# Performance work log

Measured on AMD Instinct MI355X. Metric: run time of the kernel, lower is better.

Reference implementation:

```python
import jax, jax.numpy as jnp
import numpy as np

NUM_HEADS = 16
PROJECT_DIM = 1024
HEAD_DIM = PROJECT_DIM // NUM_HEADS  # 64; used only for the softmax scale


def setup_inputs() -> dict:
    key = jax.random.key(0)
    k1, k2, k3 = jax.random.split(key, 3)
    B, N, D = 8, 3072, PROJECT_DIM
    inputs = jax.random.normal(k1, (B, N, D), dtype=jnp.float32)
    wqkv = jax.random.normal(k2, (D, 3 * D), dtype=jnp.float32) * (1.0 / np.sqrt(D))
    dense_w = jax.random.normal(k3, (3 * D, D), dtype=jnp.float32) * (1.0 / np.sqrt(3 * D))
    dense_b = jnp.zeros((D,), dtype=jnp.float32)
    return {"inputs": inputs, "wqkv": wqkv, "dense_w": dense_w, "dense_b": dense_b}


def reference(inputs, wqkv, dense_w, dense_b):
    B, N, D = inputs.shape
    H = NUM_HEADS
    # fused QKV projection: [B, N, 3D]
    qkv = jnp.einsum('bnd,de->bne', inputs, wqkv)
    # separate heads: [B, H, N, 3*head_dim]
    qkv = qkv.reshape(B, N, H, (3 * D) // H).transpose(0, 2, 1, 3)
    # NOTE: faithful to source — split along TOKEN axis (axis=2) into 3 chunks
    q, k, v = jnp.split(qkv, 3, axis=2)  # each [B, H, N//3, 3*head_dim]
    scale = 1.0 / jnp.sqrt(jnp.float32(HEAD_DIM))
    logits = jnp.einsum('bhqc,bhkc->bhqk', q, k) * scale  # [B, H, N//3, N//3]
    attn = jax.nn.softmax(logits, axis=-1)
    out = jnp.einsum('bhqk,bhkc->bhqc', attn, v)  # [B, H, N//3, 3*head_dim]
    # recombine heads -> [B, N//3, 3D]
    out = out.transpose(0, 2, 1, 3).reshape(B, N // 3, 3 * D)
    # output projection -> [B, N//3, D]
    return jnp.einsum('bnc,cd->bnd', out, dense_w) + dense_b
```

## Files before the change

### kernel.cpp

```cpp
#include <hip/hip_runtime.h>
#include <hip/hip_bf16.h>

typedef unsigned short u16;
using f32x4  = __attribute__((ext_vector_type(4))) float;
using bf16x8 = __attribute__((ext_vector_type(8))) short;

typedef __attribute__((address_space(1))) const void global_cvoid;
typedef __attribute__((address_space(3))) void lds_void;

__device__ __forceinline__ void async16(const u16* g, u16* l) {
    __builtin_amdgcn_global_load_lds((global_cvoid*)g, (lds_void*)l, 16, 0, 0);
}

__device__ __forceinline__ u16 f2bf(float f) {
    union { float f; unsigned u; } cv; cv.f = f;
    unsigned r = cv.u + 0x7fff + ((cv.u >> 16) & 1);
    return (u16)(r >> 16);
}

__device__ __forceinline__ u16 f2bf_rz(float f) {
    union { float f; unsigned u; } cv; cv.f = f;
    return (u16)(cv.u >> 16);
}

__device__ __forceinline__ float dppmax16(float x) {
    union { float f; int i; } c, o;
    c.f = x;
    o.i = __builtin_amdgcn_update_dpp(0, c.i, 0xB1,  0xF, 0xF, true); c.f = fmaxf(c.f, o.f);
    o.i = __builtin_amdgcn_update_dpp(0, c.i, 0x4E,  0xF, 0xF, true); c.f = fmaxf(c.f, o.f);
    o.i = __builtin_amdgcn_update_dpp(0, c.i, 0x141, 0xF, 0xF, true); c.f = fmaxf(c.f, o.f);
    o.i = __builtin_amdgcn_update_dpp(0, c.i, 0x140, 0xF, 0xF, true); c.f = fmaxf(c.f, o.f);
    return c.f;
}

__global__ __launch_bounds__(256) void cast_kernel(const float* __restrict__ src,
                                                   u16* __restrict__ dst, int n4) {
    int i = blockIdx.x * blockDim.x + threadIdx.x;
    int st = gridDim.x * blockDim.x;
    for (; i < n4; i += st) {
        float4 v = ((const float4*)src)[i];
        ushort4 o;
        o.x = f2bf(v.x); o.y = f2bf(v.y); o.z = f2bf(v.z); o.w = f2bf(v.w);
        ((ushort4*)dst)[i] = o;
    }
}

__global__ __launch_bounds__(256) void wtrans_kernel(const float* __restrict__ src,
                                                     u16* __restrict__ dst, int R, int C) {
    __shared__ float tile[64][68];
    int ct = blockIdx.x, rt = blockIdx.y;
    int t = threadIdx.x;
    int r = t >> 2;
    const float* s = src + (size_t)(rt * 64 + r) * C + ct * 64;
#pragma unroll
    for (int jj = 0; jj < 4; ++jj) {
        int c4 = (t & 3) + jj * 4;
        float4 v = *(const float4*)(s + c4 * 4);
        *(float4*)&tile[r][c4 * 4] = v;
    }
    __syncthreads();
    int od = t >> 2;
    u16* d = dst + (size_t)(ct * 64 + od) * R + rt * 64;
#pragma unroll
    for (int jj = 0; jj < 4; ++jj) {
        int c4 = (t & 3) + jj * 4;
        ushort4 v;
        v.x = f2bf(tile[c4 * 4 + 0][od]);
        v.y = f2bf(tile[c4 * 4 + 1][od]);
        v.z = f2bf(tile[c4 * 4 + 2][od]);
        v.w = f2bf(tile[c4 * 4 + 3][od]);
        *(ushort4*)(d + c4 * 4) = v;
    }
}

template<bool OUT_F32>
__global__ __launch_bounds__(256, 2)
void gemm_bt_kernel(const u16* __restrict__ A, const u16* __restrict__ BT,
                    void* __restrict__ Cout, const float* __restrict__ bias,
                    u16* __restrict__ VTout,
                    int M, int N, int K) {
    __shared__ u16 lA[128 * 64];
    __shared__ u16 lB[128 * 64];
    const int t = threadIdx.x;
    const int w = t >> 6, lane = t & 63;
    const int nbx = N >> 7;
    const int nwg = gridDim.x;
    int bid = blockIdx.x;
    int cpx = nwg >> 3;
    int swz = (bid & 7) * cpx + (bid >> 3);
    const int bx = swz % nbx;
    const int by = swz / nbx;
    const size_t m0 = (size_t)by * 128, n0 = (size_t)bx * 128;

    const int lr = lane >> 3;
    const int lc = (lane & 7) * 8;
    const int wr = (w >> 1) * 64, wc = (w & 1) * 64;

    f32x4 acc[4][4] = {};

    for (int kk = 0; kk < K; kk += 64) {
        __syncthreads();
#pragma unroll
        for (int i = 0; i < 4; ++i) {
            int rr = (w * 4 + i) * 8 + lr;
            async16(A  + (m0 + rr) * (size_t)K + kk + lc, &lA[(w * 4 + i) * 512]);
            async16(BT + (n0 + rr) * (size_t)K + kk + lc, &lB[(w * 4 + i) * 512]);
        }
        __syncthreads();
#pragma unroll
        for (int ks = 0; ks < 2; ++ks) {
            bf16x8 af[4], bfv[4];
#pragma unroll
            for (int m = 0; m < 4; ++m)
                af[m] = *(const bf16x8*)&lA[(wr + m * 16 + (lane & 15)) * 64 + ks * 32 + (lane >> 4) * 8];
#pragma unroll
            for (int n = 0; n < 4; ++n)
                bfv[n] = *(const bf16x8*)&lB[(wc + n * 16 + (lane & 15)) * 64 + ks * 32 + (lane >> 4) * 8];
#pragma unroll
            for (int m = 0; m < 4; ++m)
#pragma unroll
                for (int n = 0; n < 4; ++n)
                    acc[m][n] = __builtin_amdgcn_mfma_f32_16x16x32_bf16(af[m], bfv[n], acc[m][n], 0, 0, 0);
        }
    }

    const int r0 = (lane >> 4) * 4;
    const int cl = lane & 15;
    if constexpr (OUT_F32) {
        float* C = (float*)Cout;
#pragma unroll
        for (int m = 0; m < 4; ++m) {
            size_t row = m0 + wr + m * 16 + r0;
#pragma unroll
            for (int n = 0; n < 4; ++n) {
                size_t col = n0 + wc + n * 16 + cl;
                float bv = bias[col];
#pragma unroll
                for (int r = 0; r < 4; ++r)
                    C[(row + r) * (size_t)N + col] = acc[m][n][r] + bv;
            }
        }
    } else {
        u16* C = (u16*)Cout;
#pragma unroll
        for (int m = 0; m < 4; ++m) {
            size_t row = m0 + wr + m * 16 + r0;
#pragma unroll
            for (int n = 0; n < 4; ++n) {
                size_t col = n0 + wc + n * 16 + cl;
#pragma unroll
                for (int r = 0; r < 4; ++r)
                    C[(row + r) * (size_t)N + col] = f2bf(acc[m][n][r]);
            }
        }
    }
}

__global__ __launch_bounds__(512, 2)
void gemm256_kernel(const u16* __restrict__ A, const u16* __restrict__ BT,
                    u16* __restrict__ Cout, u16* __restrict__ VTout,
                    int M, int N, int K) {
    __shared__ u16 lds[65536];
    u16* lA = lds;
    u16* lB = lds + 32768;

    const int t = threadIdx.x, w = t >> 6, l = t & 63;
    const int g = l >> 4, ql = l & 15;
    const int wm = w >> 2, wn = w & 3;
    const int nbx = N >> 8;
    int bid = blockIdx.x;
    int cpx = gridDim.x >> 3;
    int swz = (bid & 7) * cpx + (bid >> 3);
    const int bx = swz % nbx, by = swz / nbx;
    const size_t m0 = (size_t)by * 256, n0 = (size_t)bx * 256;

    const u16* Ag = A  + m0 * (size_t)K;
    const u16* Bg = BT + n0 * (size_t)K;

    unsigned soff[2];
#pragma unroll
    for (int i = 0; i < 2; ++i) {
        int ch = i * 512 + t;
        int r = ch >> 2, c = ch & 3;
        soff[i] = (unsigned)(r * K + (c ^ ((r >> 1) & 3)) * 8);
    }

#define STAGE8(kh3) do {                                                           \
    int sl_ = (kh3) & 3;                                                           \
    _Pragma("unroll")                                                              \
    for (int i = 0; i < 2; ++i) {                                                  \
        async16(Ag + soff[i] + (unsigned)(kh3) * 32u, lA + sl_ * 8192 + (i * 512 + w * 64) * 8); \
        async16(Bg + soff[i] + (unsigned)(kh3) * 32u, lB + sl_ * 8192 + (i * 512 + w * 64) * 8); \
    } } while (0)

    STAGE8(0); STAGE8(1); STAGE8(2);

    f32x4 acc[8][4] = {};
    const int cswz = (g ^ ((ql >> 1) & 3)) * 8;
    const int arow = wm * 128 + ql;
    const int brow = wn * 64 + ql;

    auto phase = [&](int kh, int vm, bool st) {
        if (vm == 8)      asm volatile("s_waitcnt vmcnt(8)" ::: "memory");
        else if (vm == 4) asm volatile("s_waitcnt vmcnt(4)" ::: "memory");
        else              asm volatile("s_waitcnt vmcnt(0)" ::: "memory");
        __builtin_amdgcn_s_barrier();
        const u16* sA = lA + (kh & 3) * 8192;
        const u16* sB = lB + (kh & 3) * 8192;
        bf16x8 fa[8], fb[4];
#pragma unroll
        for (int m = 0; m < 8; ++m)
            fa[m] = *(const bf16x8*)&sA[(arow + m * 16) * 32 + cswz];
#pragma unroll
        for (int n = 0; n < 4; ++n)
            fb[n] = *(const bf16x8*)&sB[(brow + n * 16) * 32 + cswz];
        if (st) STAGE8(kh + 3);
        __builtin_amdgcn_s_setprio(1);
#pragma unroll
        for (int m = 0; m < 8; ++m)
#pragma unroll
            for (int n = 0; n < 4; ++n)
                acc[m][n] = __builtin_amdgcn_mfma_f32_16x16x32_bf16(fa[m], fb[n], acc[m][n], 0, 0, 0);
        __builtin_amdgcn_s_setprio(0);
    };

    const int KH = K >> 5;
#pragma unroll 1
    for (int kh = 0; kh < KH - 3; ++kh) phase(kh, 8, true);
    phase(KH - 3, 8, false);
    phase(KH - 2, 4, false);
    phase(KH - 1, 0, false);

    const int r0 = g * 4;
    int tok0 = (int)(m0 % 3072);
    if (tok0 >= 2048) {
        int b = (int)(m0 / 3072);
#pragma unroll
        for (int m = 0; m < 8; ++m) {
            int tok = tok0 - 2048 + wm * 128 + m * 16 + r0;
#pragma unroll
            for (int n = 0; n < 4; ++n) {
                int col = (int)n0 + wn * 64 + n * 16 + ql;
                int h = col / 192, ch = col % 192;
                ushort4 v;
                v.x = f2bf(acc[m][n][0]);
                v.y = f2bf(acc[m][n][1]);
                v.z = f2bf(acc[m][n][2]);
                v.w = f2bf(acc[m][n][3]);
                *(ushort4*)(VTout + ((size_t)(b * 16 + h) * 192 + ch) * 1024 + tok) = v;
            }
        }
    } else {
        float qs = (tok0 < 1024) ? 0.1803368801111f : 1.0f;
#pragma unroll
        for (int m = 0; m < 8; ++m) {
            size_t row = m0 + wm * 128 + m * 16 + r0;
#pragma unroll
            for (int n = 0; n < 4; ++n) {
                size_t col = n0 + wn * 64 + n * 16 + ql;
#pragma unroll
                for (int r = 0; r < 4; ++r)
                    Cout[(row + r) * (size_t)N + col] = f2bf(acc[m][n][r] * qs);
            }
        }
    }
#undef STAGE8
}

__global__ __launch_bounds__(256, 2)
void attn_kernel(const u16* __restrict__ QKV, const u16* __restrict__ VT,
                 u16* __restrict__ comb) {
    __shared__ u16 lds[40960];
    u16* lK = lds;
    u16* lV = lds + 18432;
    u16* lP = lds + 36864;

    const int t = threadIdx.x, w = t >> 6, lane = t & 63;
    const int g = lane >> 4, ql = lane & 15;
    const int bid = blockIdx.x;
    const int gid = (bid & 7) * 128 + (bid >> 3);
    const int bh = gid >> 3, qt = gid & 7;
    const int b = bh >> 4, h = bh & 15;

    const u16* Qg  = QKV + ((size_t)(b * 3072 + qt * 128 + w * 32)) * 3072 + h * 192;
    const u16* Kg  = QKV + ((size_t)(b * 3072 + 1024)) * 3072 + h * 192;
    const u16* VTg = VT + (size_t)bh * 192 * 1024;

    unsigned koff[3], voff[3];
#pragma unroll
    for (int i = 0; i < 3; ++i) {
        int ch = i * 256 + t;
        int kr = ch / 24, kc = ch % 24;
        koff[i] = kr * 3072 + (kc ^ (kr & 7)) * 8;
        int vr = ch >> 2, vc = ch & 3;
        voff[i] = vr * 1024 + (vc ^ ((vr >> 1) & 3)) * 8;
    }

#define STAGE_KV(kt) do {                                                         \
    int sl_ = (kt) % 3;                                                           \
    _Pragma("unroll")                                                             \
    for (int i = 0; i < 3; ++i) {                                                 \
        async16(Kg + koff[i] + (unsigned)(kt) * 98304u, lK + sl_ * 6144 + (i * 256 + w * 64) * 8); \
        async16(VTg + voff[i] + (unsigned)(kt) * 32u,   lV + sl_ * 6144 + (i * 256 + w * 64) * 8); \
    } } while (0)

    STAGE_KV(0);
    STAGE_KV(1);

    bf16x8 aq[2][6];
#pragma unroll
    for (int rg = 0; rg < 2; ++rg)
#pragma unroll
        for (int cs = 0; cs < 6; ++cs)
            aq[rg][cs] = *(const bf16x8*)(Qg + (size_t)(rg * 16 + ql) * 3072
                                             + cs * 32 + g * 8);

    bf16x8 vone;
#pragma unroll
    for (int j = 0; j < 8; ++j) vone[j] = (short)0x3F80;

    f32x4 acc_o[2][12] = {};
    f32x4 acc_l[2] = {};
    float m2[2] = {-1e30f, -1e30f};
    u16* lPw = &lP[w * 1024];
    const int pswz = (ql >> 2) & 3;

#pragma unroll 1
    for (int it = 0; it < 32; ++it) {
        if (it != 31) asm volatile("s_waitcnt vmcnt(6)" ::: "memory");
        else          asm volatile("s_waitcnt vmcnt(0)" ::: "memory");
        __builtin_amdgcn_s_barrier();
        if (it < 30) STAGE_KV(it + 2);

        const u16* sK = lK + (it % 3) * 6144;
        const u16* sV = lV + (it % 3) * 6144;

        f32x4 s[2][2] = {};
        __builtin_amdgcn_s_setprio(1);
#pragma unroll
        for (int kf = 0; kf < 2; ++kf) {
            const int krow = kf * 16 + ql;
#pragma unroll
            for (int cs = 0; cs < 6; ++cs) {
                bf16x8 bk = *(const bf16x8*)&sK[krow * 192 + ((cs * 4 + g) ^ (krow & 7)) * 8];
                s[0][kf] = __builtin_amdgcn_mfma_f32_16x16x32_bf16(aq[0][cs], bk, s[0][kf], 0, 0, 0);
                s[1][kf] = __builtin_amdgcn_mfma_f32_16x16x32_bf16(aq[1][cs], bk, s[1][kf], 0, 0, 0);
            }
        }
        __builtin_amdgcn_s_setprio(0);

#pragma unroll
        for (int rg = 0; rg < 2; ++rg) {
            float m = s[rg][0][0];
#pragma unroll
            for (int kf = 0; kf < 2; ++kf)
#pragma unroll
                for (int r = 0; r < 4; ++r) m = fmaxf(m, s[rg][kf][r]);
            float mx = dppmax16(m);
            bool need = mx > m2[rg] + 8.f;
            if (__any((int)need)) {
                float mn = fmaxf(m2[rg], mx);
                float fac = exp2f(m2[rg] - mn);
                m2[rg] = mn;
                acc_l[rg] *= fac;
#pragma unroll
                for (int df = 0; df < 12; ++df) acc_o[rg][df] *= fac;
            }
#pragma unroll
            for (int r = 0; r < 4; ++r) {
                int q = rg * 16 + g * 4 + r;
#pragma unroll
                for (int kf = 0; kf < 2; ++kf) {
                    float p = exp2f(s[rg][kf][r] - m2[rg]);
                    lPw[q * 32 + ((kf * 16 + ql) ^ (g << 3))] = f2bf_rz(p);
                }
            }
        }

        __builtin_amdgcn_s_setprio(1);
        {
            bf16x8 pa0 = *(const bf16x8*)&lPw[ql * 32 + ((g ^ pswz) << 3)];
            bf16x8 pa1 = *(const bf16x8*)&lPw[(16 + ql) * 32 + ((g ^ pswz) << 3)];
            acc_l[0] = __builtin_amdgcn_mfma_f32_16x16x32_bf16(pa0, vone, acc_l[0], 0, 0, 0);
            acc_l[1] = __builtin_amdgcn_mfma_f32_16x16x32_bf16(pa1, vone, acc_l[1], 0, 0, 0);
#pragma unroll
            for (int df = 0; df < 12; ++df) {
                const int vrow = df * 16 + ql;
                bf16x8 bv = *(const bf16x8*)&sV[vrow * 32 + ((g ^ ((vrow >> 1) & 3)) << 3)];
                acc_o[0][df] = __builtin_amdgcn_mfma_f32_16x16x32_bf16(pa0, bv, acc_o[0][df], 0, 0, 0);
                acc_o[1][df] = __builtin_amdgcn_mfma_f32_16x16x32_bf16(pa1, bv, acc_o[1][df], 0, 0, 0);
            }
        }
        __builtin_amdgcn_s_setprio(0);
    }

    u16* dst = comb + ((size_t)(b * 1024 + qt * 128 + w * 32)) * 3072 + h * 192;
#pragma unroll
    for (int rg = 0; rg < 2; ++rg)
#pragma unroll
        for (int r = 0; r < 4; ++r) {
            int q = rg * 16 + g * 4 + r;
            float invl = 1.0f / acc_l[rg][r];
#pragma unroll
            for (int df = 0; df < 12; ++df)
                dst[(size_t)q * 3072 + df * 16 + ql] = f2bf(acc_o[rg][df][r] * invl);
        }
#undef STAGE_KV
}

extern "C" void kernel_launch(void* const* d_in, const int* in_sizes, int n_in,
                              void* d_out, int out_size, void* d_ws, size_t ws_size,
                              hipStream_t stream) {
    const float* X  = (const float*)d_in[0];
    const float* W1 = (const float*)d_in[1];
    const float* W2 = (const float*)d_in[2];
    const float* Bb = (const float*)d_in[3];

    char* ws = (char*)d_ws;
    u16* Xb   = (u16*)(ws);
    u16* W1bT = (u16*)(ws + 50331648);
    u16* W2bT = (u16*)(ws + 56623104);
    u16* QKVb = (u16*)(ws + 62914560);
    u16* VT   = (u16*)(ws + 213909504);
    u16* comb = Xb;

    cast_kernel<<<2048, 256, 0, stream>>>(X, Xb, (8 * 3072 * 1024) / 4);
    wtrans_kernel<<<dim3(3072 / 64, 1024 / 64), 256, 0, stream>>>(W1, W1bT, 1024, 3072);
    wtrans_kernel<<<dim3(1024 / 64, 3072 / 64), 256, 0, stream>>>(W2, W2bT, 3072, 1024);
    gemm256_kernel<<<(24576 / 256) * (3072 / 256), 512, 0, stream>>>(
        Xb, W1bT, QKVb, VT, 24576, 3072, 1024);
    attn_kernel<<<1024, 256, 0, stream>>>(QKVb, VT, comb);
    gemm_bt_kernel<true><<<(8192 / 128) * (1024 / 128), 256, 0, stream>>>(
        comb, W2bT, d_out, Bb, nullptr, 8192, 1024, 3072);
}
```

Measured before the change: 386.7 us.

## Split GEMM k-step into two half phases with interleaved prefetch

```diff
diff --git a/kernel.cpp b/kernel.cpp
--- a/kernel.cpp
+++ b/kernel.cpp
@@ -185,51 +185,59 @@
         soff[i] = (unsigned)(r * K + (c ^ ((r >> 1) & 3)) * 8);
     }
 
-#define STAGE8(kh3) do {                                                           \
-    int sl_ = (kh3) & 3;                                                           \
-    _Pragma("unroll")                                                              \
-    for (int i = 0; i < 2; ++i) {                                                  \
-        async16(Ag + soff[i] + (unsigned)(kh3) * 32u, lA + sl_ * 8192 + (i * 512 + w * 64) * 8); \
-        async16(Bg + soff[i] + (unsigned)(kh3) * 32u, lB + sl_ * 8192 + (i * 512 + w * 64) * 8); \
-    } } while (0)
-
-    STAGE8(0); STAGE8(1); STAGE8(2);
+#define STAGE_PAIR(kh2, i) do {                                                    \
+    int sl_ = (kh2) & 3;                                                           \
+    async16(Ag + soff[i] + (unsigned)(kh2) * 32u, lA + sl_ * 8192 + ((i) * 512 + w * 64) * 8); \
+    async16(Bg + soff[i] + (unsigned)(kh2) * 32u, lB + sl_ * 8192 + ((i) * 512 + w * 64) * 8); \
+    } while (0)
+#define STAGE_FULL(kh2) do { STAGE_PAIR(kh2, 0); STAGE_PAIR(kh2, 1); } while (0)
+
+    STAGE_FULL(0); STAGE_FULL(1);
 
     f32x4 acc[8][4] = {};
     const int cswz = (g ^ ((ql >> 1) & 3)) * 8;
     const int arow = wm * 128 + ql;
     const int brow = wn * 64 + ql;
 
-    auto phase = [&](int kh, int vm, bool st) {
-        if (vm == 8)      asm volatile("s_waitcnt vmcnt(8)" ::: "memory");
-        else if (vm == 4) asm volatile("s_waitcnt vmcnt(4)" ::: "memory");
-        else              asm volatile("s_waitcnt vmcnt(0)" ::: "memory");
+    const int KH = K >> 5;
+#pragma unroll 1
+    for (int kh = 0; kh < KH; ++kh) {
+        if (kh < KH - 1) asm volatile("s_waitcnt vmcnt(4)" ::: "memory");
+        else             asm volatile("s_waitcnt vmcnt(0)" ::: "memory");
         __builtin_amdgcn_s_barrier();
         const u16* sA = lA + (kh & 3) * 8192;
         const u16* sB = lB + (kh & 3) * 8192;
-        bf16x8 fa[8], fb[4];
-#pragma unroll
-        for (int m = 0; m < 8; ++m)
-            fa[m] = *(const bf16x8*)&sA[(arow + m * 16) * 32 + cswz];
+
+        bf16x8 fb[4], fa[4];
 #pragma unroll
         for (int n = 0; n < 4; ++n)
             fb[n] = *(const bf16x8*)&sB[(brow + n * 16) * 32 + cswz];
-        if (st) STAGE8(kh + 3);
+#pragma unroll
+        for (int m = 0; m < 4; ++m)
+            fa[m] = *(const bf16x8*)&sA[(arow + m * 16) * 32 + cswz];
+        if (kh + 2 < KH) STAGE_PAIR(kh + 2, 0);
+        __builtin_amdgcn_s_barrier();
         __builtin_amdgcn_s_setprio(1);
 #pragma unroll
-        for (int m = 0; m < 8; ++m)
+        for (int m = 0; m < 4; ++m)
 #pragma unroll
             for (int n = 0; n < 4; ++n)
                 acc[m][n] = __builtin_amdgcn_mfma_f32_16x16x32_bf16(fa[m], fb[n], acc[m][n], 0, 0, 0);
         __builtin_amdgcn_s_setprio(0);
-    };
-
-    const int KH = K >> 5;
-#pragma unroll 1
-    for (int kh = 0; kh < KH - 3; ++kh) phase(kh, 8, true);
-    phase(KH - 3, 8, false);
-    phase(KH - 2, 4, false);
-    phase(KH - 1, 0, false);
+
+#pragma unroll
+        for (int m = 0; m < 4; ++m)
+            fa[m] = *(const bf16x8*)&sA[(arow + (m + 4) * 16) * 32 + cswz];
+        if (kh + 2 < KH) STAGE_PAIR(kh + 2, 1);
+        __builtin_amdgcn_s_barrier();
+        __builtin_amdgcn_s_setprio(1);
+#pragma unroll
+        for (int m = 0; m < 4; ++m)
+#pragma unroll
+            for (int n = 0; n < 4; ++n)
+                acc[m + 4][n] = __builtin_amdgcn_mfma_f32_16x16x32_bf16(fa[m], fb[n], acc[m + 4][n], 0, 0, 0);
+        __builtin_amdgcn_s_setprio(0);
+    }
 
     const int r0 = g * 4;
     int tok0 = (int)(m0 % 3072);
@@ -264,7 +272,8 @@
             }
         }
     }
-#undef STAGE8
+#undef STAGE_PAIR
+#undef STAGE_FULL
 }
 
 __global__ __launch_bounds__(256, 2)
```

Result: slower. 395.7 us (+2.3%).

## Shrink QKV GEMM tile to 128x256 with 4 warps and 3-stage pipeline

Applied to the files above, without the earlier changes.

```diff
diff --git a/kernel.cpp b/kernel.cpp
--- a/kernel.cpp
+++ b/kernel.cpp
@@ -156,115 +156,119 @@
     }
 }
 
-__global__ __launch_bounds__(512, 2)
-void gemm256_kernel(const u16* __restrict__ A, const u16* __restrict__ BT,
-                    u16* __restrict__ Cout, u16* __restrict__ VTout,
-                    int M, int N, int K) {
-    __shared__ u16 lds[65536];
+__global__ __launch_bounds__(256, 2)
+void gemm1_kernel(const u16* __restrict__ A, const u16* __restrict__ BT,
+                  u16* __restrict__ Cout, u16* __restrict__ VTout,
+                  int M, int N, int K) {
+    __shared__ u16 lds[36864];
     u16* lA = lds;
-    u16* lB = lds + 32768;
+    u16* lB = lds + 12288;
 
     const int t = threadIdx.x, w = t >> 6, l = t & 63;
     const int g = l >> 4, ql = l & 15;
-    const int wm = w >> 2, wn = w & 3;
+    const int wm = w >> 1, wn = w & 1;
     const int nbx = N >> 8;
     int bid = blockIdx.x;
     int cpx = gridDim.x >> 3;
     int swz = (bid & 7) * cpx + (bid >> 3);
     const int bx = swz % nbx, by = swz / nbx;
-    const size_t m0 = (size_t)by * 256, n0 = (size_t)bx * 256;
+    const size_t m0 = (size_t)by * 128, n0 = (size_t)bx * 256;
 
     const u16* Ag = A  + m0 * (size_t)K;
     const u16* Bg = BT + n0 * (size_t)K;
 
-    unsigned soff[2];
+    unsigned soffA[2], soffB[4];
 #pragma unroll
     for (int i = 0; i < 2; ++i) {
-        int ch = i * 512 + t;
+        int ch = i * 256 + t;
         int r = ch >> 2, c = ch & 3;
-        soff[i] = (unsigned)(r * K + (c ^ ((r >> 1) & 3)) * 8);
-    }
-
-#define STAGE8(kh3) do {                                                           \
-    int sl_ = (kh3) & 3;                                                           \
-    _Pragma("unroll")                                                              \
-    for (int i = 0; i < 2; ++i) {                                                  \
-        async16(Ag + soff[i] + (unsigned)(kh3) * 32u, lA + sl_ * 8192 + (i * 512 + w * 64) * 8); \
-        async16(Bg + soff[i] + (unsigned)(kh3) * 32u, lB + sl_ * 8192 + (i * 512 + w * 64) * 8); \
-    } } while (0)
-
-    STAGE8(0); STAGE8(1); STAGE8(2);
-
-    f32x4 acc[8][4] = {};
+        soffA[i] = (unsigned)(r * K + (c ^ ((r >> 1) & 3)) * 8);
+    }
+#pragma unroll
+    for (int i = 0; i < 4; ++i) {
+        int ch = i * 256 + t;
+        int r = ch >> 2, c = ch & 3;
+        soffB[i] = (unsigned)(r * K + (c ^ ((r >> 1) & 3)) * 8);
+    }
+
+#define STAGE(kt) do {                                                            \
+    int sl_ = (kt) % 3;                                                           \
+    _Pragma("unroll")                                                             \
+    for (int i = 0; i < 2; ++i)                                                   \
+        async16(Ag + soffA[i] + (unsigned)(kt) * 32u, lA + sl_ * 4096 + (i * 256 + w * 64) * 8); \
+    _Pragma("unroll")                                                             \
+    for (int i = 0; i < 4; ++i)                                                   \
+        async16(Bg + soffB[i] + (unsigned)(kt) * 32u, lB + sl_ * 8192 + (i * 256 + w * 64) * 8); \
+    } while (0)
+
+    STAGE(0);
+    STAGE(1);
+
+    f32x4 acc[4][8] = {};
     const int cswz = (g ^ ((ql >> 1) & 3)) * 8;
-    const int arow = wm * 128 + ql;
-    const int brow = wn * 64 + ql;
-
-    auto phase = [&](int kh, int vm, bool st) {
-        if (vm == 8)      asm volatile("s_waitcnt vmcnt(8)" ::: "memory");
-        else if (vm == 4) asm volatile("s_waitcnt vmcnt(4)" ::: "memory");
+    const int arow = wm * 64 + ql;
+    const int brow = wn * 128 + ql;
+
+    const int KT = K >> 5;
+#pragma unroll 1
+    for (int it = 0; it < KT; ++it) {
+        if (it != KT - 1) asm volatile("s_waitcnt vmcnt(6)" ::: "memory");
         else              asm volatile("s_waitcnt vmcnt(0)" ::: "memory");
         __builtin_amdgcn_s_barrier();
-        const u16* sA = lA + (kh & 3) * 8192;
-        const u16* sB = lB + (kh & 3) * 8192;
-        bf16x8 fa[8], fb[4];
-#pragma unroll
-        for (int m = 0; m < 8; ++m)
-            fa[m] = *(const bf16x8*)&sA[(arow + m * 16) * 32 + cswz];
-#pragma unroll
-        for (int n = 0; n < 4; ++n)
-            fb[n] = *(const bf16x8*)&sB[(brow + n * 16) * 32 + cswz];
-        if (st) STAGE8(kh + 3);
+        if (it + 2 < KT) STAGE(it + 2);
+
+        const u16* sA = lA + (it % 3) * 4096;
+        const u16* sB = lB + (it % 3) * 8192;
+        bf16x8 fa[4], fb[8];
+#pragma unroll
+        for (int mf = 0; mf < 4; ++mf)
+            fa[mf] = *(const bf16x8*)&sA[(arow + mf * 16) * 32 + cswz];
+#pragma unroll
+        for (int nf = 0; nf < 8; ++nf)
+            fb[nf] = *(const bf16x8*)&sB[(brow + nf * 16) * 32 + cswz];
         __builtin_amdgcn_s_setprio(1);
 #pragma unroll
-        for (int m = 0; m < 8; ++m)
-#pragma unroll
-            for (int n = 0; n < 4; ++n)
-                acc[m][n] = __builtin_amdgcn_mfma_f32_16x16x32_bf16(fa[m], fb[n], acc[m][n], 0, 0, 0);
+        for (int mf = 0; mf < 4; ++mf)
+#pragma unroll
+            for (int nf = 0; nf < 8; ++nf)
+                acc[mf][nf] = __builtin_amdgcn_mfma_f32_16x16x32_bf16(fa[mf], fb[nf], acc[mf][nf], 0, 0, 0);
         __builtin_amdgcn_s_setprio(0);
-    };
-
-    const int KH = K >> 5;
-#pragma unroll 1
-    for (int kh = 0; kh < KH - 3; ++kh) phase(kh, 8, true);
-    phase(KH - 3, 8, false);
-    phase(KH - 2, 4, false);
-    phase(KH - 1, 0, false);
+    }
 
     const int r0 = g * 4;
     int tok0 = (int)(m0 % 3072);
     if (tok0 >= 2048) {
         int b = (int)(m0 / 3072);
 #pragma unroll
-        for (int m = 0; m < 8; ++m) {
-            int tok = tok0 - 2048 + wm * 128 + m * 16 + r0;
-#pragma unroll
-            for (int n = 0; n < 4; ++n) {
-                int col = (int)n0 + wn * 64 + n * 16 + ql;
+        for (int mf = 0; mf < 4; ++mf) {
+            int tok = tok0 - 2048 + wm * 64 + mf * 16 + r0;
+#pragma unroll
+            for (int nf = 0; nf < 8; ++nf) {
+                int col = (int)n0 + wn * 128 + nf * 16 + ql;
                 int h = col / 192, ch = col % 192;
                 ushort4 v;
-                v.x = f2bf(acc[m][n][0]);
-                v.y = f2bf(acc[m][n][1]);
-                v.z = f2bf(acc[m][n][2]);
-                v.w = f2bf(acc[m][n][3]);
+                v.x = f2bf(acc[mf][nf][0]);
+                v.y = f2bf(acc[mf][nf][1]);
+                v.z = f2bf(acc[mf][nf][2]);
+                v.w = f2bf(acc[mf][nf][3]);
                 *(ushort4*)(VTout + ((size_t)(b * 16 + h) * 192 + ch) * 1024 + tok) = v;
             }
         }
     } else {
         float qs = (tok0 < 1024) ? 0.1803368801111f : 1.0f;
 #pragma unroll
-        for (int m = 0; m < 8; ++m) {
-            size_t row = m0 + wm * 128 + m * 16 + r0;
-#pragma unroll
-            for (int n = 0; n < 4; ++n) {
-                size_t col = n0 + wn * 64 + n * 16 + ql;
+        for (int mf = 0; mf < 4; ++mf) {
+            size_t row = m0 + wm * 64 + mf * 16 + r0;
+#pragma unroll
+            for (int nf = 0; nf < 8; ++nf) {
+                size_t col = n0 + wn * 128 + nf * 16 + ql;
 #pragma unroll
                 for (int r = 0; r < 4; ++r)
-                    Cout[(row + r) * (size_t)N + col] = f2bf(acc[m][n][r] * qs);
-            }
-        }
-    }
-#undef STAGE8
+                    Cout[(row + r) * (size_t)N + col] = f2bf(acc[mf][nf][r] * qs);
+            }
+        }
+    }
+#undef STAGE
 }
 
 __global__ __launch_bounds__(256, 2)
@@ -427,7 +431,7 @@
     cast_kernel<<<2048, 256, 0, stream>>>(X, Xb, (8 * 3072 * 1024) / 4);
     wtrans_kernel<<<dim3(3072 / 64, 1024 / 64), 256, 0, stream>>>(W1, W1bT, 1024, 3072);
     wtrans_kernel<<<dim3(1024 / 64, 3072 / 64), 256, 0, stream>>>(W2, W2bT, 3072, 1024);
-    gemm256_kernel<<<(24576 / 256) * (3072 / 256), 512, 0, stream>>>(
+    gemm1_kernel<<<(24576 / 128) * (3072 / 256), 256, 0, stream>>>(
         Xb, W1bT, QKVb, VT, 24576, 3072, 1024);
     attn_kernel<<<1024, 256, 0, stream>>>(QKVb, VT, comb);
     gemm_bt_kernel<true><<<(8192 / 128) * (1024 / 128), 256, 0, stream>>>(
```

Result: slower. 397.1 us (+2.7%).
